# Kernel tuning notes

Hardware: AMD Instinct MI355X
Metric: run time of the kernel (lower is better)

The kernel has to match this reference:

```python
import jax, jax.numpy as jnp
import numpy as np
import math

DT = 1024
HID = 512
B, M, N = 16, 1024, 1024
NEG_INF = -1.0e9


def _linear(x, w, b):
    # torch nn.Linear convention: w is (out, in)
    return x @ w.T + b


def setup_inputs() -> dict:
    key = jax.random.key(0)
    ks = jax.random.split(key, 20)
    s = 0.02
    inp = {
        "oV": jax.random.normal(ks[0], (B, M, DT), jnp.float32),
        "oT": jax.random.normal(ks[1], (B, N, DT), jnp.float32),
        "Wq_v_w": jax.random.normal(ks[2], (DT, DT), jnp.float32) * s,
        "Wq_v_b": jnp.zeros((DT,), jnp.float32),
        "Wk_t_w": jax.random.normal(ks[3], (DT, DT), jnp.float32) * s,
        "Wk_t_b": jnp.zeros((DT,), jnp.float32),
        "Wv_t_w": jax.random.normal(ks[4], (DT, DT), jnp.float32) * s,
        "Wv_t_b": jnp.zeros((DT,), jnp.float32),
        "Wq_t_w": jax.random.normal(ks[5], (DT, DT), jnp.float32) * s,
        "Wq_t_b": jnp.zeros((DT,), jnp.float32),
        "Wk_v_w": jax.random.normal(ks[6], (DT, DT), jnp.float32) * s,
        "Wk_v_b": jnp.zeros((DT,), jnp.float32),
        "Wv_v_w": jax.random.normal(ks[7], (DT, DT), jnp.float32) * s,
        "Wv_v_b": jnp.zeros((DT,), jnp.float32),
        "ffn1_w": jax.random.normal(ks[8], (HID, 2 * DT), jnp.float32) * s,
        "ffn1_b": jnp.zeros((HID,), jnp.float32),
        "ffn2_w": jax.random.normal(ks[9], (1, HID), jnp.float32) * s,
        "ffn2_b": jnp.zeros((1,), jnp.float32),
    }
    return inp


def reference(oV, oT, Wq_v_w, Wq_v_b, Wk_t_w, Wk_t_b, Wv_t_w, Wv_t_b,
              Wq_t_w, Wq_t_b, Wk_v_w, Wk_v_b, Wv_v_w, Wv_v_b,
              ffn1_w, ffn1_b, ffn2_w, ffn2_b):
    dt = oV.shape[-1]
    inv_sqrt = 1.0 / math.sqrt(dt)

    # shared similarity-derived mask
    sim_raw = jnp.einsum('bmd,bnd->bmn', oV, oT)            # (B, m, n)
    v_pool = oV.mean(axis=1)                                  # (B, dt)
    t_pool = oT.mean(axis=1)                                  # (B, dt)
    h = jax.nn.relu(_linear(jnp.concatenate([v_pool, t_pool], axis=-1), ffn1_w, ffn1_b))
    l = jax.nn.sigmoid(_linear(h, ffn2_w, ffn2_b))[:, 0]      # (B,)
    S = jax.nn.softmax(sim_raw * inv_sqrt, axis=-1)
    Mmask = S >= l[:, None, None]                             # (B, m, n) bool

    # V -> T masked cross-attention
    Q_v = _linear(oV, Wq_v_w, Wq_v_b)
    K_t = _linear(oT, Wk_t_w, Wk_t_b)
    V_t = _linear(oT, Wv_t_w, Wv_t_b)
    scores_vt = jnp.einsum('bmd,bnd->bmn', Q_v, K_t) * inv_sqrt
    attn_vt = jax.nn.softmax(jnp.where(Mmask, scores_vt, NEG_INF), axis=-1)
    out_vt = jnp.einsum('bmn,bnd->bmd', attn_vt, V_t)

    # T -> V masked cross-attention (transposed mask)
    Q_t = _linear(oT, Wq_t_w, Wq_t_b)
    K_v = _linear(oV, Wk_v_w, Wk_v_b)
    V_v = _linear(oV, Wv_v_w, Wv_v_b)
    scores_tv = jnp.einsum('bnd,bmd->bnm', Q_t, K_v) * inv_sqrt
    attn_tv = jax.nn.softmax(jnp.where(Mmask.transpose(0, 2, 1), scores_tv, NEG_INF), axis=-1)
    out_tv = jnp.einsum('bnm,bmd->bnd', attn_tv, V_v)

    return out_vt, out_tv, Mmask.astype(jnp.float32)
```

## Files before the change

### kernel.cpp

```cpp
#include <hip/hip_runtime.h>
#include <stdint.h>

typedef unsigned short u16;
typedef unsigned char  u8;
typedef unsigned int   u32;
typedef __attribute__((ext_vector_type(8))) short  short8;
typedef __attribute__((ext_vector_type(4))) float  floatx4;

#define Bz   16
#define Mm   1024
#define Nn   1024
#define Dd   1024
#define HIDh 512
#define INV_SQRT_D 0.03125f
#define NEGINF (-1.0e9f)
#define BMDc  ((size_t)Bz * Mm * Dd)
#define sMDc  ((long)Mm * Dd)

__device__ __forceinline__ float bf2f(u16 h) {
    union { u32 u; float f; } c; c.u = ((u32)h) << 16; return c.f;
}
__device__ __forceinline__ u16 f2bf(float f) {
    union { float f; u32 u; } c; c.f = f;
    u32 u = c.u;
    return (u16)((u + 0x7FFFu + ((u >> 16) & 1u)) >> 16);
}
__device__ __forceinline__ void g2lds16(const u16* g, u16* l) {
    __builtin_amdgcn_global_load_lds((const __attribute__((address_space(1))) void*)g,
                                     (__attribute__((address_space(3))) void*)l, 16, 0, 0);
}

__device__ __forceinline__ float waveSum(float v) {
#pragma unroll
    for (int o = 32; o > 0; o >>= 1) v += __shfl_xor(v, o);
    return v;
}
__device__ __forceinline__ float waveMax(float v) {
#pragma unroll
    for (int o = 32; o > 0; o >>= 1) v = fmaxf(v, __shfl_xor(v, o));
    return v;
}

template <bool OUT_FP32, bool BIAS, bool TRANSC>
__global__ __launch_bounds__(512, 2) void gemm256(
    const u16* __restrict__ A, const u16* __restrict__ Bm,
    const float* __restrict__ bias, void* __restrict__ Cv,
    int K, int ldc, long sA, long sB, long sC)
{
    __shared__ __align__(16) u16 lds[2][2][256 * 64];
    const int tid  = threadIdx.x;
    const int lane = tid & 63;
    const int wv   = tid >> 6;
    const int wr   = wv >> 2;
    const int wc   = wv & 3;
    const int fr   = lane & 15, fq = lane >> 4;

    const int gX = gridDim.x, gY = gridDim.y;
    int bid = blockIdx.x + gX * (blockIdx.y + gY * blockIdx.z);
    const int nwg = gX * gY * gridDim.z;
    int wg = (bid & 7) * (nwg >> 3) + (bid >> 3);
    const int bx = wg % gX; wg /= gX;
    const int by = wg % gY;
    const int bz = wg / gY;

    const long tileM = (long)bx * 256, tileN = (long)by * 256;
    A  += (long)bz * sA;
    Bm += (long)bz * sB;
    const int T = K >> 6;

    floatx4 acc[8][4];
#pragma unroll
    for (int i = 0; i < 8; ++i)
#pragma unroll
        for (int j = 0; j < 4; ++j) acc[i][j] = (floatx4){0.f, 0.f, 0.f, 0.f};

    const int lrow = lane >> 3;
    const int scol = ((lane & 7) ^ lrow) << 3;
    const int sw   = fr & 7;
    const int kc0  = ((fq ^ sw) << 3);
    const int kc1  = (((4 + fq) ^ sw) << 3);

    auto stage = [&](int tt, int side, int hh, int bb) {
#pragma unroll
        for (int i = 0; i < 2; ++i) {
            const int j = i * 8 + wv;
            const int prow = side ? (((j >> 2) << 6) + (hh << 5) + ((j & 3) << 3))
                                  : (((j >> 3) << 7) + (hh << 6) + ((j & 7) << 3));
            const u16* src = side ? Bm : A;
            const long rb  = side ? tileN : tileM;
            g2lds16(src + (size_t)(rb + prow + lrow) * (size_t)K + (size_t)(tt << 6) + scol,
                    &lds[bb][side][prow * 64]);
        }
    };

    short8 Af[4][2], Bf[4][2];
    auto quad = [&](int mb, int nb) {
#pragma unroll
        for (int m = 0; m < 4; ++m)
#pragma unroll
            for (int n = 0; n < 2; ++n) {
                acc[mb + m][nb + n] = __builtin_amdgcn_mfma_f32_16x16x32_bf16(
                    Af[m][0], Bf[nb + n][0], acc[mb + m][nb + n], 0, 0, 0);
                acc[mb + m][nb + n] = __builtin_amdgcn_mfma_f32_16x16x32_bf16(
                    Af[m][1], Bf[nb + n][1], acc[mb + m][nb + n], 0, 0, 0);
            }
    };

    stage(0, 0, 0, 0); stage(0, 1, 0, 0); stage(0, 1, 1, 0); stage(0, 0, 1, 0);
    stage(1, 0, 0, 1); stage(1, 1, 1, 1); stage(1, 0, 1, 1);
    asm volatile("s_waitcnt vmcnt(6)" ::: "memory");
    __builtin_amdgcn_s_barrier();

    for (int t = 0; t < T; ++t) {
        const int cb = t & 1;
        const u16* lA = &lds[cb][0][0];
        const u16* lB = &lds[cb][1][0];

#pragma unroll
        for (int m = 0; m < 4; ++m) {
            const int ro = ((wr << 7) + (m << 4) + fr) * 64;
            Af[m][0] = *(const short8*)&lA[ro + kc0];
            Af[m][1] = *(const short8*)&lA[ro + kc1];
        }
#pragma unroll
        for (int n = 0; n < 2; ++n) {
            const int ro = ((wc << 6) + (n << 4) + fr) * 64;
            Bf[n][0] = *(const short8*)&lB[ro + kc0];
            Bf[n][1] = *(const short8*)&lB[ro + kc1];
        }
        if (t + 1 < T) stage(t + 1, 1, 0, cb ^ 1);
        asm volatile("" ::: "memory");
        __builtin_amdgcn_s_barrier();
        asm volatile("s_waitcnt lgkmcnt(0)" ::: "memory");
        __builtin_amdgcn_sched_barrier(0);
        __builtin_amdgcn_s_setprio(1);
        quad(0, 0);
        __builtin_amdgcn_s_setprio(0);
        asm volatile("" ::: "memory");
        __builtin_amdgcn_s_barrier();

#pragma unroll
        for (int n = 2; n < 4; ++n) {
            const int ro = ((wc << 6) + (n << 4) + fr) * 64;
            Bf[n][0] = *(const short8*)&lB[ro + kc0];
            Bf[n][1] = *(const short8*)&lB[ro + kc1];
        }
        if (t + 2 < T) stage(t + 2, 0, 0, cb);
        asm volatile("" ::: "memory");
        __builtin_amdgcn_s_barrier();
        asm volatile("s_waitcnt lgkmcnt(0)" ::: "memory");
        __builtin_amdgcn_sched_barrier(0);
        __builtin_amdgcn_s_setprio(1);
        quad(0, 2);
        __builtin_amdgcn_s_setprio(0);
        asm volatile("" ::: "memory");
        __builtin_amdgcn_s_barrier();

#pragma unroll
        for (int m = 0; m < 4; ++m) {
            const int ro = ((wr << 7) + ((m + 4) << 4) + fr) * 64;
            Af[m][0] = *(const short8*)&lA[ro + kc0];
            Af[m][1] = *(const short8*)&lA[ro + kc1];
        }
        if (t + 2 < T) stage(t + 2, 1, 1, cb);
        asm volatile("" ::: "memory");
        __builtin_amdgcn_s_barrier();
        asm volatile("s_waitcnt lgkmcnt(0)" ::: "memory");
        __builtin_amdgcn_sched_barrier(0);
        __builtin_amdgcn_s_setprio(1);
        quad(4, 2);
        __builtin_amdgcn_s_setprio(0);
        asm volatile("" ::: "memory");
        __builtin_amdgcn_s_barrier();

        if (t + 2 < T) stage(t + 2, 0, 1, cb);
        asm volatile("" ::: "memory");
        __builtin_amdgcn_s_barrier();
        __builtin_amdgcn_s_setprio(1);
        quad(4, 0);
        __builtin_amdgcn_s_setprio(0);
        if (t + 1 < T) {
            if (t + 2 < T) asm volatile("s_waitcnt vmcnt(6)" ::: "memory");
            else           asm volatile("s_waitcnt vmcnt(0)" ::: "memory");
        }
        asm volatile("" ::: "memory");
        __builtin_amdgcn_s_barrier();
    }

#pragma unroll
    for (int j = 0; j < 4; ++j) {
        const long col = tileN + (wc << 6) + (j << 4) + fr;
        float bv = 0.f;
        if constexpr (BIAS) bv = bias[col];
#pragma unroll
        for (int i = 0; i < 8; ++i) {
            const long row0 = tileM + (wr << 7) + (i << 4) + (fq << 2);
#pragma unroll
            for (int r = 0; r < 4; ++r) {
                const float v = acc[i][j][r] + bv;
                const long row = row0 + r;
                if constexpr (OUT_FP32) {
                    ((float*)Cv + (long)bz * sC)[row * ldc + col] = v;
                } else if constexpr (TRANSC) {
                    const long b = row >> 10, mloc = row & 1023;
                    ((u16*)Cv)[b * sMDc + col * Mm + mloc] = f2bf(v);
                } else {
                    ((u16*)Cv + (long)bz * sC)[row * ldc + col] = f2bf(v);
                }
            }
        }
    }
}

__global__ __launch_bounds__(512, 2) void gemm_proj3(
    const u16* __restrict__ A, const u16* __restrict__ Bm,
    const float* __restrict__ bcat,
    u16* __restrict__ Pq, u16* __restrict__ Pk, u16* __restrict__ Pv, int K)
{
    __shared__ __align__(16) u16 lds[2][2][256 * 64];
    const int tid  = threadIdx.x;
    const int lane = tid & 63;
    const int wv   = tid >> 6;
    const int wr   = wv >> 2;
    const int wc   = wv & 3;
    const int fr   = lane & 15, fq = lane >> 4;

    const int gX = gridDim.x, gY = gridDim.y;
    int bid = blockIdx.x + gX * blockIdx.y;
    const int nwg = gX * gY;
    int wg = (bid & 7) * (nwg >> 3) + (bid >> 3);
    const int bx = wg % gX;
    const int by = wg / gX;

    const long tileM = (long)bx * 256, tileN = (long)by * 256;
    const int T = K >> 6;

    floatx4 acc[8][4];
#pragma unroll
    for (int i = 0; i < 8; ++i)
#pragma unroll
        for (int j = 0; j < 4; ++j) acc[i][j] = (floatx4){0.f, 0.f, 0.f, 0.f};

    const int lrow = lane >> 3;
    const int scol = ((lane & 7) ^ lrow) << 3;
    const int sw   = fr & 7;
    const int kc0  = ((fq ^ sw) << 3);
    const int kc1  = (((4 + fq) ^ sw) << 3);

    auto stage = [&](int tt, int side, int hh, int bb) {
#pragma unroll
        for (int i = 0; i < 2; ++i) {
            const int j = i * 8 + wv;
            const int prow = side ? (((j >> 2) << 6) + (hh << 5) + ((j & 3) << 3))
                                  : (((j >> 3) << 7) + (hh << 6) + ((j & 7) << 3));
            const u16* src = side ? Bm : A;
            const long rb  = side ? tileN : tileM;
            g2lds16(src + (size_t)(rb + prow + lrow) * (size_t)K + (size_t)(tt << 6) + scol,
                    &lds[bb][side][prow * 64]);
        }
    };

    short8 Af[4][2], Bf[4][2];
    auto quad = [&](int mb, int nb) {
#pragma unroll
        for (int m = 0; m < 4; ++m)
#pragma unroll
            for (int n = 0; n < 2; ++n) {
                acc[mb + m][nb + n] = __builtin_amdgcn_mfma_f32_16x16x32_bf16(
                    Af[m][0], Bf[nb + n][0], acc[mb + m][nb + n], 0, 0, 0);
                acc[mb + m][nb + n] = __builtin_amdgcn_mfma_f32_16x16x32_bf16(
                    Af[m][1], Bf[nb + n][1], acc[mb + m][nb + n], 0, 0, 0);
            }
    };

    stage(0, 0, 0, 0); stage(0, 1, 0, 0); stage(0, 1, 1, 0); stage(0, 0, 1, 0);
    stage(1, 0, 0, 1); stage(1, 1, 1, 1); stage(1, 0, 1, 1);
    asm volatile("s_waitcnt vmcnt(6)" ::: "memory");
    __builtin_amdgcn_s_barrier();

    for (int t = 0; t < T; ++t) {
        const int cb = t & 1;
        const u16* lA = &lds[cb][0][0];
        const u16* lB = &lds[cb][1][0];

#pragma unroll
        for (int m = 0; m < 4; ++m) {
            const int ro = ((wr << 7) + (m << 4) + fr) * 64;
            Af[m][0] = *(const short8*)&lA[ro + kc0];
            Af[m][1] = *(const short8*)&lA[ro + kc1];
        }
#pragma unroll
        for (int n = 0; n < 2; ++n) {
            const int ro = ((wc << 6) + (n << 4) + fr) * 64;
            Bf[n][0] = *(const short8*)&lB[ro + kc0];
            Bf[n][1] = *(const short8*)&lB[ro + kc1];
        }
        if (t + 1 < T) stage(t + 1, 1, 0, cb ^ 1);
        asm volatile("" ::: "memory");
        __builtin_amdgcn_s_barrier();
        asm volatile("s_waitcnt lgkmcnt(0)" ::: "memory");
        __builtin_amdgcn_sched_barrier(0);
        __builtin_amdgcn_s_setprio(1);
        quad(0, 0);
        __builtin_amdgcn_s_setprio(0);
        asm volatile("" ::: "memory");
        __builtin_amdgcn_s_barrier();

#pragma unroll
        for (int n = 2; n < 4; ++n) {
            const int ro = ((wc << 6) + (n << 4) + fr) * 64;
            Bf[n][0] = *(const short8*)&lB[ro + kc0];
            Bf[n][1] = *(const short8*)&lB[ro + kc1];
        }
        if (t + 2 < T) stage(t + 2, 0, 0, cb);
        asm volatile("" ::: "memory");
        __builtin_amdgcn_s_barrier();
        asm volatile("s_waitcnt lgkmcnt(0)" ::: "memory");
        __builtin_amdgcn_sched_barrier(0);
        __builtin_amdgcn_s_setprio(1);
        quad(0, 2);
        __builtin_amdgcn_s_setprio(0);
        asm volatile("" ::: "memory");
        __builtin_amdgcn_s_barrier();

#pragma unroll
        for (int m = 0; m < 4; ++m) {
            const int ro = ((wr << 7) + ((m + 4) << 4) + fr) * 64;
            Af[m][0] = *(const short8*)&lA[ro + kc0];
            Af[m][1] = *(const short8*)&lA[ro + kc1];
        }
        if (t + 2 < T) stage(t + 2, 1, 1, cb);
        asm volatile("" ::: "memory");
        __builtin_amdgcn_s_barrier();
        asm volatile("s_waitcnt lgkmcnt(0)" ::: "memory");
        __builtin_amdgcn_sched_barrier(0);
        __builtin_amdgcn_s_setprio(1);
        quad(4, 2);
        __builtin_amdgcn_s_setprio(0);
        asm volatile("" ::: "memory");
        __builtin_amdgcn_s_barrier();

        if (t + 2 < T) stage(t + 2, 0, 1, cb);
        asm volatile("" ::: "memory");
        __builtin_amdgcn_s_barrier();
        __builtin_amdgcn_s_setprio(1);
        quad(4, 0);
        __builtin_amdgcn_s_setprio(0);
        if (t + 1 < T) {
            if (t + 2 < T) asm volatile("s_waitcnt vmcnt(6)" ::: "memory");
            else           asm volatile("s_waitcnt vmcnt(0)" ::: "memory");
        }
        asm volatile("" ::: "memory");
        __builtin_amdgcn_s_barrier();
    }

#pragma unroll
    for (int j = 0; j < 4; ++j) {
        const long colL = tileN + (wc << 6) + (j << 4) + fr;
        const int oid = (int)(colL >> 10);
        const long col = colL & 1023;
        const float bv = bcat[colL];
#pragma unroll
        for (int i = 0; i < 8; ++i) {
            const long row0 = tileM + (wr << 7) + (i << 4) + (fq << 2);
#pragma unroll
            for (int r = 0; r < 4; ++r) {
                const float v = acc[i][j][r] + bv;
                const long row = row0 + r;
                if (oid == 0)      Pq[row * Dd + col] = f2bf(v);
                else if (oid == 1) Pk[row * Dd + col] = f2bf(v);
                else { const long b = row >> 10, mloc = row & 1023;
                       Pv[b * sMDc + col * Mm + mloc] = f2bf(v); }
            }
        }
    }
}

__global__ __launch_bounds__(256) void conv_pool(
    const float* __restrict__ oV, const float* __restrict__ oT,
    u16* __restrict__ oVb, u16* __restrict__ oTb,
    float* __restrict__ vpool, float* __restrict__ tpool)
{
    const int b = blockIdx.y, srci = blockIdx.z;
    const float* src = (srci ? oT : oV) + (size_t)b * Mm * Dd;
    u16* dst = (srci ? oTb : oVb) + (size_t)b * Mm * Dd;
    const int c4 = threadIdx.x * 4;
    const int r0 = blockIdx.x * 64;
    float4 s = {0.f, 0.f, 0.f, 0.f};
    for (int r = r0; r < r0 + 64; ++r) {
        const float4 v = *(const float4*)&src[(size_t)r * Dd + c4];
        s.x += v.x; s.y += v.y; s.z += v.z; s.w += v.w;
        ushort4 o;
        o.x = f2bf(v.x); o.y = f2bf(v.y); o.z = f2bf(v.z); o.w = f2bf(v.w);
        *(ushort4*)&dst[(size_t)r * Dd + c4] = o;
    }
    float* pool = (srci ? tpool : vpool) + (size_t)b * Dd + c4;
    atomicAdd(pool + 0, s.x * (1.0f / Mm));
    atomicAdd(pool + 1, s.y * (1.0f / Mm));
    atomicAdd(pool + 2, s.z * (1.0f / Mm));
    atomicAdd(pool + 3, s.w * (1.0f / Mm));
}

__global__ __launch_bounds__(256) void wconv6(
    const float* __restrict__ w0, const float* __restrict__ w1, const float* __restrict__ w2,
    const float* __restrict__ w3, const float* __restrict__ w4, const float* __restrict__ w5,
    u16* __restrict__ dst)
{
    const float* src;
    switch (blockIdx.y) {
        case 0: src = w0; break; case 1: src = w1; break; case 2: src = w2; break;
        case 3: src = w3; break; case 4: src = w4; break; default: src = w5; break;
    }
    const size_t i = (size_t)blockIdx.x * 256 + threadIdx.x;
    const float4 a = ((const float4*)src)[2 * i];
    const float4 b = ((const float4*)src)[2 * i + 1];
    short8 o;
    o[0]=(short)f2bf(a.x); o[1]=(short)f2bf(a.y); o[2]=(short)f2bf(a.z); o[3]=(short)f2bf(a.w);
    o[4]=(short)f2bf(b.x); o[5]=(short)f2bf(b.y); o[6]=(short)f2bf(b.z); o[7]=(short)f2bf(b.w);
    *(short8*)(dst + (((size_t)blockIdx.y) << 20) + 8 * i) = o;
}

__global__ __launch_bounds__(256) void bcat_kernel(
    const float* __restrict__ b0, const float* __restrict__ b1, const float* __restrict__ b2,
    const float* __restrict__ b3, const float* __restrict__ b4, const float* __restrict__ b5,
    float* __restrict__ out)
{
    const int i = blockIdx.x * 256 + threadIdx.x;
    const int seg = i >> 10;
    const float* s;
    switch (seg) {
        case 0: s = b0; break; case 1: s = b1; break; case 2: s = b2; break;
        case 3: s = b3; break; case 4: s = b4; break; default: s = b5; break;
    }
    out[i] = s[i & 1023];
}

__global__ __launch_bounds__(256) void ffn1_kernel(
    const float* __restrict__ vpool, const float* __restrict__ tpool,
    const float* __restrict__ f1w, const float* __restrict__ f1b,
    float* __restrict__ hbuf)
{
    const int j = blockIdx.x, b = blockIdx.y;
    const int t = threadIdx.x, wv = t >> 6, lane = t & 63;
    __shared__ float red[4];
    const float* w = f1w + (size_t)j * (2 * Dd);
    float a = 0.f;
    for (int k = t; k < Dd; k += 256) a += vpool[b * Dd + k] * w[k];
    for (int k = t; k < Dd; k += 256) a += tpool[b * Dd + k] * w[Dd + k];
    a = waveSum(a);
    if (lane == 0) red[wv] = a;
    __syncthreads();
    if (t == 0) hbuf[b * HIDh + j] = fmaxf(red[0] + red[1] + red[2] + red[3] + f1b[j], 0.0f);
}

__global__ __launch_bounds__(256) void ffn2_kernel(
    const float* __restrict__ hbuf, const float* __restrict__ f2w,
    const float* __restrict__ f2b, float* __restrict__ lbuf)
{
    const int b = blockIdx.x;
    const int t = threadIdx.x, wv = t >> 6, lane = t & 63;
    __shared__ float red[4];
    float p = 0.f;
    for (int j = t; j < HIDh; j += 256) p += hbuf[b * HIDh + j] * f2w[j];
    p = waveSum(p);
    if (lane == 0) red[wv] = p;
    __syncthreads();
    if (t == 0) {
        const float z = red[0] + red[1] + red[2] + red[3] + f2b[0];
        lbuf[b] = 1.0f / (1.0f + expf(-z));
    }
}

__global__ __launch_bounds__(256) void sim_softmax_mask(
    const u16* __restrict__ scores, const float* __restrict__ lbuf, float* __restrict__ maskF)
{
    const int row = blockIdx.x, b = blockIdx.y;
    const int t = threadIdx.x, wv = t >> 6, lane = t & 63;
    __shared__ float red[8];
    const size_t off = ((size_t)b * Mm + row) * Nn;
    const uint2 sv = *(const uint2*)(scores + off + 4 * t);
    const float x0 = bf2f((u16)(sv.x & 0xFFFFu)) * INV_SQRT_D;
    const float x1 = bf2f((u16)(sv.x >> 16))     * INV_SQRT_D;
    const float x2 = bf2f((u16)(sv.y & 0xFFFFu)) * INV_SQRT_D;
    const float x3 = bf2f((u16)(sv.y >> 16))     * INV_SQRT_D;
    float mx = waveMax(fmaxf(fmaxf(x0, x1), fmaxf(x2, x3)));
    if (lane == 0) red[wv] = mx;
    __syncthreads();
    mx = fmaxf(fmaxf(red[0], red[1]), fmaxf(red[2], red[3]));
    const float e0 = expf(x0 - mx), e1 = expf(x1 - mx), e2 = expf(x2 - mx), e3 = expf(x3 - mx);
    float s = waveSum(e0 + e1 + e2 + e3);
    if (lane == 0) red[4 + wv] = s;
    __syncthreads();
    const float inv = 1.0f / fmaxf(red[4] + red[5] + red[6] + red[7], 1e-30f);
    const float l = lbuf[b];
    float4 mk;
    mk.x = (e0 * inv >= l) ? 1.0f : 0.0f;
    mk.y = (e1 * inv >= l) ? 1.0f : 0.0f;
    mk.z = (e2 * inv >= l) ? 1.0f : 0.0f;
    mk.w = (e3 * inv >= l) ? 1.0f : 0.0f;
    *(float4*)(maskF + off + 4 * t) = mk;
}

__global__ __launch_bounds__(256) void transpose_mask(
    const float* __restrict__ maskF, u8* __restrict__ maskT)
{
    __shared__ u8 tile[64][68];
    const int m0 = blockIdx.x * 64, n0 = blockIdx.y * 64, b = blockIdx.z;
    const int t = threadIdx.x;
    const int r = t >> 2, c = (t & 3) * 16;
    const float* src = maskF + ((size_t)b * Mm + (m0 + r)) * Nn + n0 + c;
    float4 f0 = ((const float4*)src)[0];
    float4 f1 = ((const float4*)src)[1];
    float4 f2 = ((const float4*)src)[2];
    float4 f3 = ((const float4*)src)[3];
    u8* dst = &tile[r][c];
    dst[0]=f0.x!=0.f; dst[1]=f0.y!=0.f; dst[2]=f0.z!=0.f; dst[3]=f0.w!=0.f;
    dst[4]=f1.x!=0.f; dst[5]=f1.y!=0.f; dst[6]=f1.z!=0.f; dst[7]=f1.w!=0.f;
    dst[8]=f2.x!=0.f; dst[9]=f2.y!=0.f; dst[10]=f2.z!=0.f; dst[11]=f2.w!=0.f;
    dst[12]=f3.x!=0.f; dst[13]=f3.y!=0.f; dst[14]=f3.z!=0.f; dst[15]=f3.w!=0.f;
    __syncthreads();
    union { u8 b[16]; uint4 v; } pk;
#pragma unroll
    for (int k = 0; k < 16; ++k) pk.b[k] = tile[c + k][r];
    *(uint4*)(maskT + ((size_t)b * Nn + (n0 + r)) * Mm + m0 + c) = pk.v;
}

template <bool TRANSP>
__global__ __launch_bounds__(256) void masked_softmax(
    u16* __restrict__ scores, const float* __restrict__ maskF, const u8* __restrict__ maskT)
{
    const int row = blockIdx.x, b = blockIdx.y;
    const int t = threadIdx.x, wv = t >> 6, lane = t & 63;
    __shared__ float red[8];
    const size_t off = ((size_t)b * Mm + row) * Nn;
    const uint2 sv = *(const uint2*)(scores + off + 4 * t);
    float x0 = bf2f((u16)(sv.x & 0xFFFFu)) * INV_SQRT_D;
    float x1 = bf2f((u16)(sv.x >> 16))     * INV_SQRT_D;
    float x2 = bf2f((u16)(sv.y & 0xFFFFu)) * INV_SQRT_D;
    float x3 = bf2f((u16)(sv.y >> 16))     * INV_SQRT_D;
    if (TRANSP) {
        const u32 mk = *(const u32*)(maskT + off + 4 * t);
        if (!(mk & 0x000000FFu)) x0 = NEGINF;
        if (!(mk & 0x0000FF00u)) x1 = NEGINF;
        if (!(mk & 0x00FF0000u)) x2 = NEGINF;
        if (!(mk & 0xFF000000u)) x3 = NEGINF;
    } else {
        const float4 mk = *(const float4*)(maskF + off + 4 * t);
        if (mk.x == 0.f) x0 = NEGINF;
        if (mk.y == 0.f) x1 = NEGINF;
        if (mk.z == 0.f) x2 = NEGINF;
        if (mk.w == 0.f) x3 = NEGINF;
    }
    float mx = waveMax(fmaxf(fmaxf(x0, x1), fmaxf(x2, x3)));
    if (lane == 0) red[wv] = mx;
    __syncthreads();
    mx = fmaxf(fmaxf(red[0], red[1]), fmaxf(red[2], red[3]));
    const float e0 = expf(x0 - mx), e1 = expf(x1 - mx), e2 = expf(x2 - mx), e3 = expf(x3 - mx);
    float s = waveSum(e0 + e1 + e2 + e3);
    if (lane == 0) red[4 + wv] = s;
    __syncthreads();
    const float inv = 1.0f / fmaxf(red[4] + red[5] + red[6] + red[7], 1e-30f);
    uint2 pk;
    pk.x = (u32)f2bf(e0 * inv) | ((u32)f2bf(e1 * inv) << 16);
    pk.y = (u32)f2bf(e2 * inv) | ((u32)f2bf(e3 * inv) << 16);
    *(uint2*)(scores + off + 4 * t) = pk;
}

extern "C" void kernel_launch(void* const* d_in, const int* in_sizes, int n_in,
                              void* d_out, int out_size, void* d_ws, size_t ws_size,
                              hipStream_t stream)
{
    (void)in_sizes; (void)n_in; (void)out_size; (void)ws_size;
    const float* oV     = (const float*)d_in[0];
    const float* oT     = (const float*)d_in[1];
    const float* Wq_v_w = (const float*)d_in[2];
    const float* Wq_v_b = (const float*)d_in[3];
    const float* Wk_t_w = (const float*)d_in[4];
    const float* Wk_t_b = (const float*)d_in[5];
    const float* Wv_t_w = (const float*)d_in[6];
    const float* Wv_t_b = (const float*)d_in[7];
    const float* Wq_t_w = (const float*)d_in[8];
    const float* Wq_t_b = (const float*)d_in[9];
    const float* Wk_v_w = (const float*)d_in[10];
    const float* Wk_v_b = (const float*)d_in[11];
    const float* Wv_v_w = (const float*)d_in[12];
    const float* Wv_v_b = (const float*)d_in[13];
    const float* f1w    = (const float*)d_in[14];
    const float* f1b    = (const float*)d_in[15];
    const float* f2w    = (const float*)d_in[16];
    const float* f2b    = (const float*)d_in[17];

    float* out_vt = (float*)d_out;
    float* out_tv = out_vt + BMDc;
    float* maskF  = out_vt + 2 * BMDc;

    u16* S0a = (u16*)d_ws;
    u16* S1a = S0a + BMDc;
    u16* S2a = S1a + BMDc;
    u16* S0b = S2a + BMDc;
    u16* S1b = S0b + BMDc;
    u16* S2b = S1b + BMDc;
    u16* S3  = S2b + BMDc;
    u16* oVb = S3 + BMDc;
    u16* oTb = oVb + BMDc;
    u16* Wc  = oTb + BMDc;
    u8*  maskT = (u8*)(Wc + 6 * (1 << 20));
    float* bcat  = (float*)(maskT + BMDc);
    float* vpool = bcat + 6144;
    float* tpool = vpool + Bz * Dd;
    float* hbuf  = tpool + Bz * Dd;
    float* lbuf  = hbuf + Bz * HIDh;

    const dim3 blk(256), blk512(512);
    const dim3 gBat(Mm / 256, Nn / 256, Bz);
    const dim3 gFproj(Bz * Mm / 256, 3 * Dd / 256, 1);
    const dim3 gRow(Mm, Bz);
    const dim3 gTrp(Mm / 64, Nn / 64, Bz);
    const long sMD = sMDc, sMN = (long)Mm * Nn;

    wconv6<<<dim3(512, 6), blk, 0, stream>>>(Wq_v_w, Wk_v_w, Wv_v_w, Wq_t_w, Wk_t_w, Wv_t_w, Wc);
    bcat_kernel<<<dim3(24), blk, 0, stream>>>(Wq_v_b, Wk_v_b, Wv_v_b, Wq_t_b, Wk_t_b, Wv_t_b, bcat);

    hipMemsetAsync(vpool, 0, 2 * Bz * Dd * sizeof(float), stream);
    conv_pool<<<dim3(16, Bz, 2), blk, 0, stream>>>(oV, oT, oVb, oTb, vpool, tpool);
    ffn1_kernel<<<dim3(HIDh, Bz), blk, 0, stream>>>(vpool, tpool, f1w, f1b, hbuf);
    ffn2_kernel<<<dim3(Bz), blk, 0, stream>>>(hbuf, f2w, f2b, lbuf);

    gemm256<false,false,false><<<gBat, blk512, 0, stream>>>(oVb, oTb, nullptr, S3, Dd, Nn, sMD, sMD, sMN);
    sim_softmax_mask<<<gRow, blk, 0, stream>>>(S3, lbuf, maskF);
    transpose_mask<<<gTrp, blk, 0, stream>>>(maskF, maskT);

    gemm_proj3<<<gFproj, blk512, 0, stream>>>(oVb, Wc,                bcat,        S0a, S1b, S2b, Dd);
    gemm_proj3<<<gFproj, blk512, 0, stream>>>(oTb, Wc + 3 * (1 << 20), bcat + 3072, S0b, S1a, S2a, Dd);

    gemm256<false,false,false><<<gBat, blk512, 0, stream>>>(S0a, S1a, nullptr, S3, Dd, Nn, sMD, sMD, sMN);
    masked_softmax<false><<<gRow, blk, 0, stream>>>(S3, maskF, maskT);
    gemm256<true ,false,false><<<gBat, blk512, 0, stream>>>(S3, S2a, nullptr, out_vt, Nn, Dd, sMN, sMD, sMD);

    gemm256<false,false,false><<<gBat, blk512, 0, stream>>>(S0b, S1b, nullptr, S3, Dd, Nn, sMD, sMD, sMN);
    masked_softmax<true><<<gRow, blk, 0, stream>>>(S3, maskF, maskT);
    gemm256<true ,false,false><<<gBat, blk512, 0, stream>>>(S3, S2b, nullptr, out_tv, Nn, Dd, sMN, sMD, sMD);
}
```

Baseline: 1.011 ms.

## Stage GEMM epilogues through LDS for coalesced vector stores; remap proj tile order

GEMM epilogues now write accumulators into LDS, then store full rows with 16-byte vector writes instead of scattered 2- and 4-byte stores. The projection kernel's transposed V output is packed and XOR-swizzled in LDS so the column-major writes also coalesce. The projection grid gets a hand-written tile remap that groups workgroups into blocks, aimed at better L2 reuse. This adds extra barriers and LDS traffic in the epilogue, and the fp32 path needs two passes because the tile does not fit in LDS at once.

```diff
diff --git a/kernel.cpp b/kernel.cpp
--- a/kernel.cpp
+++ b/kernel.cpp
@@ -4,6 +4,7 @@
 typedef unsigned short u16;
 typedef unsigned char  u8;
 typedef unsigned int   u32;
+typedef unsigned long long u64;
 typedef __attribute__((ext_vector_type(8))) short  short8;
 typedef __attribute__((ext_vector_type(4))) float  floatx4;
 
@@ -41,11 +42,10 @@
     return v;
 }
 
-template <bool OUT_FP32, bool BIAS, bool TRANSC>
+template <bool OUT_FP32>
 __global__ __launch_bounds__(512, 2) void gemm256(
     const u16* __restrict__ A, const u16* __restrict__ Bm,
-    const float* __restrict__ bias, void* __restrict__ Cv,
-    int K, int ldc, long sA, long sB, long sC)
+    void* __restrict__ Cv, int K, int ldc, long sA, long sB, long sC)
 {
     __shared__ __align__(16) u16 lds[2][2][256 * 64];
     const int tid  = threadIdx.x;
@@ -187,26 +187,55 @@
         __builtin_amdgcn_s_barrier();
     }
 
-#pragma unroll
-    for (int j = 0; j < 4; ++j) {
-        const long col = tileN + (wc << 6) + (j << 4) + fr;
-        float bv = 0.f;
-        if constexpr (BIAS) bv = bias[col];
-#pragma unroll
-        for (int i = 0; i < 8; ++i) {
-            const long row0 = tileM + (wr << 7) + (i << 4) + (fq << 2);
-#pragma unroll
-            for (int r = 0; r < 4; ++r) {
-                const float v = acc[i][j][r] + bv;
-                const long row = row0 + r;
-                if constexpr (OUT_FP32) {
-                    ((float*)Cv + (long)bz * sC)[row * ldc + col] = v;
-                } else if constexpr (TRANSC) {
-                    const long b = row >> 10, mloc = row & 1023;
-                    ((u16*)Cv)[b * sMDc + col * Mm + mloc] = f2bf(v);
-                } else {
-                    ((u16*)Cv + (long)bz * sC)[row * ldc + col] = f2bf(v);
+    __syncthreads();
+    if constexpr (!OUT_FP32) {
+        u16* l2 = (u16*)&lds[0][0][0];
+#pragma unroll
+        for (int j = 0; j < 4; ++j) {
+            const int col = (wc << 6) + (j << 4) + fr;
+#pragma unroll
+            for (int i = 0; i < 8; ++i) {
+                const int row0 = (wr << 7) + (i << 4) + (fq << 2);
+#pragma unroll
+                for (int r = 0; r < 4; ++r)
+                    l2[(row0 + r) * 256 + col] = f2bf(acc[i][j][r]);
+            }
+        }
+        __syncthreads();
+        u16* C = (u16*)Cv + (long)bz * sC;
+#pragma unroll
+        for (int it = 0; it < 16; ++it) {
+            const int row = it * 16 + (tid >> 5);
+            const int ch  = tid & 31;
+            const short8 v = *(const short8*)&l2[row * 256 + ch * 8];
+            *(short8*)&C[(tileM + row) * (long)ldc + tileN + ch * 8] = v;
+        }
+    } else {
+        float* l2f = (float*)&lds[0][0][0];
+        float* C = (float*)Cv + (long)bz * sC;
+#pragma unroll
+        for (int pass = 0; pass < 2; ++pass) {
+            if (pass) __syncthreads();
+            if (wr == pass) {
+#pragma unroll
+                for (int j = 0; j < 4; ++j) {
+                    const int col = (wc << 6) + (j << 4) + fr;
+#pragma unroll
+                    for (int i = 0; i < 8; ++i) {
+                        const int row0 = (i << 4) + (fq << 2);
+#pragma unroll
+                        for (int r = 0; r < 4; ++r)
+                            l2f[(row0 + r) * 256 + col] = acc[i][j][r];
+                    }
                 }
+            }
+            __syncthreads();
+#pragma unroll
+            for (int it = 0; it < 16; ++it) {
+                const int row = it * 8 + (tid >> 6);
+                const int ch  = tid & 63;
+                const float4 v = *(const float4*)&l2f[row * 256 + ch * 4];
+                *(float4*)&C[(tileM + pass * 128 + row) * (long)ldc + tileN + ch * 4] = v;
             }
         }
     }
@@ -225,12 +254,14 @@
     const int wc   = wv & 3;
     const int fr   = lane & 15, fq = lane >> 4;
 
-    const int gX = gridDim.x, gY = gridDim.y;
-    int bid = blockIdx.x + gX * blockIdx.y;
-    const int nwg = gX * gY;
-    int wg = (bid & 7) * (nwg >> 3) + (bid >> 3);
-    const int bx = wg % gX;
-    const int by = wg / gX;
+    const int bid = blockIdx.x + 64 * blockIdx.y;
+    const int x  = bid & 7, l = bid >> 3;
+    const int x0 = (x & 3) * 16, y0 = (x >> 2) * 6;
+    const int w = l >> 5, r = l & 31;
+    int bx, by;
+    if (w == 0)      { bx = x0 + (r & 7);      by = y0 + (r >> 3); }
+    else if (w == 1) { bx = x0 + 8 + (r & 7);  by = y0 + (r >> 3); }
+    else             { bx = x0 + (r & 15);     by = y0 + 4 + (r >> 4); }
 
     const long tileM = (long)bx * 256, tileN = (long)by * 256;
     const int T = K >> 6;
@@ -354,24 +385,58 @@
         __builtin_amdgcn_s_barrier();
     }
 
-#pragma unroll
-    for (int j = 0; j < 4; ++j) {
-        const long colL = tileN + (wc << 6) + (j << 4) + fr;
-        const int oid = (int)(colL >> 10);
-        const long col = colL & 1023;
-        const float bv = bcat[colL];
-#pragma unroll
-        for (int i = 0; i < 8; ++i) {
-            const long row0 = tileM + (wr << 7) + (i << 4) + (fq << 2);
-#pragma unroll
-            for (int r = 0; r < 4; ++r) {
-                const float v = acc[i][j][r] + bv;
-                const long row = row0 + r;
-                if (oid == 0)      Pq[row * Dd + col] = f2bf(v);
-                else if (oid == 1) Pk[row * Dd + col] = f2bf(v);
-                else { const long b = row >> 10, mloc = row & 1023;
-                       Pv[b * sMDc + col * Mm + mloc] = f2bf(v); }
+    const int oid = (int)(tileN >> 10);
+    __syncthreads();
+    if (oid < 2) {
+        u16* l2 = (u16*)&lds[0][0][0];
+#pragma unroll
+        for (int j = 0; j < 4; ++j) {
+            const int col = (wc << 6) + (j << 4) + fr;
+            const float bv = bcat[tileN + col];
+#pragma unroll
+            for (int i = 0; i < 8; ++i) {
+                const int row0 = (wr << 7) + (i << 4) + (fq << 2);
+#pragma unroll
+                for (int r = 0; r < 4; ++r)
+                    l2[(row0 + r) * 256 + col] = f2bf(acc[i][j][r] + bv);
             }
+        }
+        __syncthreads();
+        u16* P = oid ? Pk : Pq;
+        const long colN = tileN & 1023;
+#pragma unroll
+        for (int it = 0; it < 16; ++it) {
+            const int row = it * 16 + (tid >> 5);
+            const int ch  = tid & 31;
+            const short8 v = *(const short8*)&l2[row * 256 + ch * 8];
+            *(short8*)&P[(tileM + row) * (long)Dd + colN + ch * 8] = v;
+        }
+    } else {
+        char* l2c = (char*)&lds[0][0][0];
+#pragma unroll
+        for (int j = 0; j < 4; ++j) {
+            const int col = (wc << 6) + (j << 4) + fr;
+            const float bv = bcat[tileN + col];
+            const int swz = (col & 7) << 4;
+#pragma unroll
+            for (int i = 0; i < 8; ++i) {
+                const int row0 = (wr << 7) + (i << 4) + (fq << 2);
+                const u64 pk = (u64)f2bf(acc[i][j][0] + bv)
+                             | ((u64)f2bf(acc[i][j][1] + bv) << 16)
+                             | ((u64)f2bf(acc[i][j][2] + bv) << 32)
+                             | ((u64)f2bf(acc[i][j][3] + bv) << 48);
+                *(u64*)(l2c + col * 512 + ((row0 * 2) ^ swz)) = pk;
+            }
+        }
+        __syncthreads();
+        const long b  = tileM >> 10, tm = tileM & 1023;
+        const long colN = tileN & 1023;
+#pragma unroll
+        for (int it = 0; it < 16; ++it) {
+            const int col = it * 16 + (tid >> 5);
+            const int ch  = tid & 31;
+            const short8 v = *(const short8*)(l2c + col * 512 + ((ch * 16) ^ ((col & 7) << 4)));
+            *(short8*)&Pv[b * sMDc + (colN + col) * (long)Mm + tm + ch * 8] = v;
         }
     }
 }
@@ -613,7 +678,7 @@
 
     const dim3 blk(256), blk512(512);
     const dim3 gBat(Mm / 256, Nn / 256, Bz);
-    const dim3 gFproj(Bz * Mm / 256, 3 * Dd / 256, 1);
+    const dim3 gFproj(64, 12, 1);
     const dim3 gRow(Mm, Bz);
     const dim3 gTrp(Mm / 64, Nn / 64, Bz);
     const long sMD = sMDc, sMN = (long)Mm * Nn;
@@ -626,18 +691,18 @@
     ffn1_kernel<<<dim3(HIDh, Bz), blk, 0, stream>>>(vpool, tpool, f1w, f1b, hbuf);
     ffn2_kernel<<<dim3(Bz), blk, 0, stream>>>(hbuf, f2w, f2b, lbuf);
 
-    gemm256<false,false,false><<<gBat, blk512, 0, stream>>>(oVb, oTb, nullptr, S3, Dd, Nn, sMD, sMD, sMN);
+    gemm256<false><<<gBat, blk512, 0, stream>>>(oVb, oTb, S3, Dd, Nn, sMD, sMD, sMN);
     sim_softmax_mask<<<gRow, blk, 0, stream>>>(S3, lbuf, maskF);
     transpose_mask<<<gTrp, blk, 0, stream>>>(maskF, maskT);
 
-    gemm_proj3<<<gFproj, blk512, 0, stream>>>(oVb, Wc,                bcat,        S0a, S1b, S2b, Dd);
+    gemm_proj3<<<gFproj, blk512, 0, stream>>>(oVb, Wc,                 bcat,        S0a, S1b, S2b, Dd);
     gemm_proj3<<<gFproj, blk512, 0, stream>>>(oTb, Wc + 3 * (1 << 20), bcat + 3072, S0b, S1a, S2a, Dd);
 
-    gemm256<false,false,false><<<gBat, blk512, 0, stream>>>(S0a, S1a, nullptr, S3, Dd, Nn, sMD, sMD, sMN);
+    gemm256<false><<<gBat, blk512, 0, stream>>>(S0a, S1a, S3, Dd, Nn, sMD, sMD, sMN);
     masked_softmax<false><<<gRow, blk, 0, stream>>>(S3, maskF, maskT);
-    gemm256<true ,false,false><<<gBat, blk512, 0, stream>>>(S3, S2a, nullptr, out_vt, Nn, Dd, sMN, sMD, sMD);
-
-    gemm256<false,false,false><<<gBat, blk512, 0, stream>>>(S0b, S1b, nullptr, S3, Dd, Nn, sMD, sMD, sMN);
+    gemm256<true ><<<gBat, blk512, 0, stream>>>(S3, S2a, out_vt, Nn, Dd, sMN, sMD, sMD);
+
+    gemm256<false><<<gBat, blk512, 0, stream>>>(S0b, S1b, S3, Dd, Nn, sMD, sMD, sMN);
     masked_softmax<true><<<gRow, blk, 0, stream>>>(S3, maskF, maskT);
-    gemm256<true ,false,false><<<gBat, blk512, 0, stream>>>(S3, S2b, nullptr, out_tv, Nn, Dd, sMN, sMD, sMD);
-}
+    gemm256<true ><<<gBat, blk512, 0, stream>>>(S3, S2b, out_tv, Nn, Dd, sMN, sMD, sMD);
+}
```

New measurement: 826.7 us. 1.22x faster.
